# Optimization experiments

Hardware: AMD Instinct MI355X
Metric: run time of the kernel (lower is better)

Reference implementation:

```python
import jax, jax.numpy as jnp
import numpy as np

NUM_BINS = 100
EPS = 1e-6  # F.pairwise_distance default eps (added to the difference)


def setup_inputs() -> dict:
    key = jax.random.key(0)
    k0, k1, k2 = jax.random.split(key, 3)
    n, c, h, w = 1, 32, 1024, 1024
    # scale so per-pixel L2 distances (~sqrt(2c)*0.05 ~ 0.4) fall inside histc's [0,1]
    feat_t0 = jax.random.normal(k0, (n, c, h, w), dtype=jnp.float32) * 0.05
    feat_t1 = jax.random.normal(k1, (n, c, h, w), dtype=jnp.float32) * 0.05
    ground_truth = jax.random.randint(k2, (n, h, w), 0, 2, dtype=jnp.int32)
    return {"feat_t0": feat_t0, "feat_t1": feat_t1, "ground_truth": ground_truth}


def _masked_hist(d, mask):
    # torch.histc(x, bins=100, min=0, max=1): values outside [0,1] ignored,
    # right edge (==1) goes into last bin.
    in_range = (d >= 0.0) & (d <= 1.0)
    bins = jnp.clip(jnp.floor(d * NUM_BINS).astype(jnp.int32), 0, NUM_BINS - 1)
    wts = (mask & in_range).astype(d.dtype)
    return jnp.zeros((NUM_BINS,), d.dtype).at[bins].add(wts)


def reference(feat_t0, feat_t1, ground_truth):
    n, c, h, w = feat_t0.shape
    # view(c, h*w).T -> [h*w, c] pixel vectors (matches original's n=1 assumption)
    x0 = feat_t0.reshape(c, h * w).T
    x1 = feat_t1.reshape(c, h * w).T
    # F.pairwise_distance p=2: ||x0 - x1 + eps||_2 over channel dim -> [h*w]
    d = jnp.sqrt(jnp.sum((x0 - x1 + EPS) ** 2, axis=1))

    gt = ground_truth.reshape(h * w)
    pos_mask = gt == 0
    neg_mask = jnp.logical_not(pos_mask)
    pos_size = jnp.sum(pos_mask).astype(d.dtype)
    neg_size = jnp.sum(neg_mask).astype(d.dtype)

    hist_pos = _masked_hist(d, pos_mask) / pos_size
    hist_neg = _masked_hist(d, neg_mask) / neg_size

    # F.kl_div(input=hist_pos, target=hist_neg), reduction='mean':
    # mean over bins of target*(log(target) - input); target==0 contributes 0.
    pointwise = jnp.where(hist_neg > 0,
                          hist_neg * (jnp.log(jnp.where(hist_neg > 0, hist_neg, 1.0)) - hist_pos),
                          0.0)
    kl = jnp.mean(pointwise)
    loss = 1.0 + kl  # dist = 1.0/1 + kl
    return loss
```

## Files before the change

kernel.cpp:

```cpp
#include <hip/hip_runtime.h>
#include <math.h>

#define NUM_BINS 100
#define EPS 1e-6f

#define WS_WORDS (2 * NUM_BINS + 1)

#define NREP 8
#define SH_POSC (2 * NUM_BINS * NREP)
#define SH_WORDS (SH_POSC + 1)

typedef float  vfloat4 __attribute__((ext_vector_type(4)));
typedef int    vint4   __attribute__((ext_vector_type(4)));

__global__ void hml_init_ws(unsigned int* __restrict__ ws) {
    int i = blockIdx.x * blockDim.x + threadIdx.x;
    if (i < WS_WORDS) ws[i] = 0u;
}

__global__ __launch_bounds__(256) void hml_hist32(
    const vfloat4* __restrict__ f0v, const vfloat4* __restrict__ f1v,
    const vint4* __restrict__ gt, unsigned int* __restrict__ ws, int hw4)
{
    __shared__ unsigned int sh[SH_WORDS];
    for (int i = threadIdx.x; i < SH_WORDS; i += 256) sh[i] = 0u;
    __syncthreads();

    const int idx = blockIdx.x * 256 + threadIdx.x;
    const int col = threadIdx.x & (NREP - 1);

    vint4 g = __builtin_nontemporal_load(&gt[idx]);
    float s0 = 0.f, s1 = 0.f, s2 = 0.f, s3 = 0.f;

    #pragma unroll 1
    for (int cg = 0; cg < 32; cg += 4) {
        vfloat4 a[4], b[4];
        #pragma unroll
        for (int j = 0; j < 4; ++j)
            a[j] = __builtin_nontemporal_load(&f0v[(size_t)(cg + j) * hw4 + idx]);
        #pragma unroll
        for (int j = 0; j < 4; ++j)
            b[j] = __builtin_nontemporal_load(&f1v[(size_t)(cg + j) * hw4 + idx]);
        #pragma unroll
        for (int j = 0; j < 4; ++j) {
            float e0 = a[j].x - b[j].x + EPS;
            float e1 = a[j].y - b[j].y + EPS;
            float e2 = a[j].z - b[j].z + EPS;
            float e3 = a[j].w - b[j].w + EPS;
            s0 = fmaf(e0, e0, s0);
            s1 = fmaf(e1, e1, s1);
            s2 = fmaf(e2, e2, s2);
            s3 = fmaf(e3, e3, s3);
        }
    }

    float d[4] = { sqrtf(s0), sqrtf(s1), sqrtf(s2), sqrtf(s3) };
    int gg[4] = { g.x, g.y, g.z, g.w };

    int posc = (gg[0] == 0) + (gg[1] == 0) + (gg[2] == 0) + (gg[3] == 0);
    for (int off = 32; off > 0; off >>= 1)
        posc += __shfl_down(posc, off, 64);
    if ((threadIdx.x & 63) == 0 && posc)
        atomicAdd(&sh[SH_POSC], (unsigned)posc);

    #pragma unroll
    for (int k = 0; k < 4; ++k) {
        float dd = d[k];
        if (dd <= 1.0f) {
            int bin = (int)(dd * (float)NUM_BINS);
            if (bin > NUM_BINS - 1) bin = NUM_BINS - 1;
            int logical = bin + ((gg[k] != 0) ? NUM_BINS : 0);
            atomicAdd(&sh[logical * NREP + col], 1u);
        }
    }

    __syncthreads();
    {
        int i = threadIdx.x;
        if (i < 2 * NUM_BINS) {
            unsigned v = 0;
            #pragma unroll
            for (int c = 0; c < NREP; ++c) v += sh[i * NREP + c];
            if (v) atomicAdd(&ws[i], v);
        } else if (i == 2 * NUM_BINS) {
            unsigned v = sh[SH_POSC];
            if (v) atomicAdd(&ws[2 * NUM_BINS], v);
        }
    }
}

__global__ __launch_bounds__(256) void hml_hist_generic(
    const float* __restrict__ f0, const float* __restrict__ f1,
    const int* __restrict__ gt, unsigned int* __restrict__ ws,
    int hw, int C)
{
    __shared__ unsigned int sh[WS_WORDS];
    for (int i = threadIdx.x; i < WS_WORDS; i += blockDim.x) sh[i] = 0u;
    __syncthreads();

    const int hw4 = hw >> 2;
    const int idx = blockIdx.x * blockDim.x + threadIdx.x;

    if (idx < hw4) {
        const float4* __restrict__ f0v = (const float4*)f0;
        const float4* __restrict__ f1v = (const float4*)f1;
        float s0 = 0.f, s1 = 0.f, s2 = 0.f, s3 = 0.f;
        for (int c = 0; c < C; ++c) {
            float4 a = f0v[(size_t)c * hw4 + idx];
            float4 b = f1v[(size_t)c * hw4 + idx];
            float e0 = a.x - b.x + EPS, e1 = a.y - b.y + EPS;
            float e2 = a.z - b.z + EPS, e3 = a.w - b.w + EPS;
            s0 = fmaf(e0, e0, s0); s1 = fmaf(e1, e1, s1);
            s2 = fmaf(e2, e2, s2); s3 = fmaf(e3, e3, s3);
        }
        int4 g = ((const int4*)gt)[idx];
        float d[4] = { sqrtf(s0), sqrtf(s1), sqrtf(s2), sqrtf(s3) };
        int gg[4] = { g.x, g.y, g.z, g.w };
        int posc = 0;
        #pragma unroll
        for (int k = 0; k < 4; ++k) {
            posc += (gg[k] == 0) ? 1 : 0;
            float dd = d[k];
            if (dd <= 1.0f) {
                int bin = (int)(dd * (float)NUM_BINS);
                if (bin > NUM_BINS - 1) bin = NUM_BINS - 1;
                atomicAdd(&sh[bin + ((gg[k] != 0) ? NUM_BINS : 0)], 1u);
            }
        }
        if (posc) atomicAdd(&sh[2 * NUM_BINS], (unsigned)posc);
    }
    __syncthreads();
    for (int i = threadIdx.x; i < WS_WORDS; i += blockDim.x) {
        unsigned v = sh[i];
        if (v) atomicAdd(&ws[i], v);
    }
}

__global__ void hml_final(const unsigned int* __restrict__ ws,
                          float* __restrict__ out, int hw)
{
    __shared__ float terms[NUM_BINS];
    int i = threadIdx.x;
    unsigned pos = ws[2 * NUM_BINS];
    float pos_size = (float)pos;
    float neg_size = (float)(hw - (int)pos);
    if (i < NUM_BINS) {
        float hp = (float)ws[i] / pos_size;
        unsigned cn = ws[NUM_BINS + i];
        float hn = (float)cn / neg_size;
        terms[i] = (cn > 0u) ? hn * (logf(hn) - hp) : 0.0f;
    }
    __syncthreads();
    if (i == 0) {
        float s = 0.f;
        for (int k = 0; k < NUM_BINS; ++k) s += terms[k];
        out[0] = 1.0f + s / (float)NUM_BINS;
    }
}

extern "C" void kernel_launch(void* const* d_in, const int* in_sizes, int n_in,
                              void* d_out, int out_size, void* d_ws, size_t ws_size,
                              hipStream_t stream) {
    const float* f0 = (const float*)d_in[0];
    const float* f1 = (const float*)d_in[1];
    const int*   gt = (const int*)d_in[2];
    float* out = (float*)d_out;
    unsigned int* ws = (unsigned int*)d_ws;

    const int hw = in_sizes[2];
    const int C  = in_sizes[0] / hw;

    hml_init_ws<<<1, 256, 0, stream>>>(ws);

    if (C == 32 && (hw & 1023) == 0) {
        const int hw4 = hw >> 2;
        const int blocks = hw4 / 256;
        hml_hist32<<<blocks, 256, 0, stream>>>(
            (const vfloat4*)f0, (const vfloat4*)f1, (const vint4*)gt, ws, hw4);
    } else {
        const int hw4 = hw >> 2;
        const int blocks = (hw4 + 255) / 256;
        hml_hist_generic<<<blocks, 256, 0, stream>>>(f0, f1, gt, ws, hw, C);
    }

    hml_final<<<1, 128, 0, stream>>>(ws, out, hw);
}
```

Measured before the change: 259.7 us.

## Replace global atomics with per-block partial histograms reduced in final kernel

Each histogram block now writes its 201-word partial result to its own workspace slice instead of doing global atomicAdds on a shared histogram. The final kernel, widened to 1024 threads, sums the slices across all 1024 blocks before computing the KL term. This removes the init kernel launch and contention on the global atomics. In exchange it adds a serial reduction over about 200K words in a single block, and the workspace must be large enough to hold all slices.

```diff
diff --git a/kernel.cpp b/kernel.cpp
--- a/kernel.cpp
+++ b/kernel.cpp
@@ -4,7 +4,7 @@
 #define NUM_BINS 100
 #define EPS 1e-6f
 
-#define WS_WORDS (2 * NUM_BINS + 1)
+#define SLICE_WORDS (2 * NUM_BINS + 1)
 
 #define NREP 8
 #define SH_POSC (2 * NUM_BINS * NREP)
@@ -12,11 +12,6 @@
 
 typedef float  vfloat4 __attribute__((ext_vector_type(4)));
 typedef int    vint4   __attribute__((ext_vector_type(4)));
-
-__global__ void hml_init_ws(unsigned int* __restrict__ ws) {
-    int i = blockIdx.x * blockDim.x + threadIdx.x;
-    if (i < WS_WORDS) ws[i] = 0u;
-}
 
 __global__ __launch_bounds__(256) void hml_hist32(
     const vfloat4* __restrict__ f0v, const vfloat4* __restrict__ f1v,
@@ -77,14 +72,14 @@
     __syncthreads();
     {
         int i = threadIdx.x;
+        size_t base = (size_t)blockIdx.x * SLICE_WORDS;
         if (i < 2 * NUM_BINS) {
             unsigned v = 0;
             #pragma unroll
             for (int c = 0; c < NREP; ++c) v += sh[i * NREP + c];
-            if (v) atomicAdd(&ws[i], v);
+            ws[base + i] = v;
         } else if (i == 2 * NUM_BINS) {
-            unsigned v = sh[SH_POSC];
-            if (v) atomicAdd(&ws[2 * NUM_BINS], v);
+            ws[base + i] = sh[SH_POSC];
         }
     }
 }
@@ -94,8 +89,8 @@
     const int* __restrict__ gt, unsigned int* __restrict__ ws,
     int hw, int C)
 {
-    __shared__ unsigned int sh[WS_WORDS];
-    for (int i = threadIdx.x; i < WS_WORDS; i += blockDim.x) sh[i] = 0u;
+    __shared__ unsigned int sh[SLICE_WORDS];
+    for (int i = threadIdx.x; i < SLICE_WORDS; i += blockDim.x) sh[i] = 0u;
     __syncthreads();
 
     const int hw4 = hw >> 2;
@@ -130,28 +125,44 @@
         if (posc) atomicAdd(&sh[2 * NUM_BINS], (unsigned)posc);
     }
     __syncthreads();
-    for (int i = threadIdx.x; i < WS_WORDS; i += blockDim.x) {
-        unsigned v = sh[i];
-        if (v) atomicAdd(&ws[i], v);
-    }
+    for (int i = threadIdx.x; i < SLICE_WORDS; i += blockDim.x)
+        ws[(size_t)blockIdx.x * SLICE_WORDS + i] = sh[i];
 }
 
-__global__ void hml_final(const unsigned int* __restrict__ ws,
-                          float* __restrict__ out, int hw)
+__global__ __launch_bounds__(1024) void hml_final(
+    const unsigned int* __restrict__ ws, float* __restrict__ out,
+    int hw, int nblocks)
 {
+    __shared__ unsigned int part[4][SLICE_WORDS];
     __shared__ float terms[NUM_BINS];
-    int i = threadIdx.x;
-    unsigned pos = ws[2 * NUM_BINS];
+    const int t = threadIdx.x;
+    const int word = t & 255;
+    const int q = t >> 8;
+
+    if (word < SLICE_WORDS) {
+        unsigned acc = 0;
+        #pragma unroll 4
+        for (int b = q; b < nblocks; b += 4)
+            acc += ws[(size_t)b * SLICE_WORDS + word];
+        part[q][word] = acc;
+    }
+    __syncthreads();
+
+    if (t < SLICE_WORDS)
+        part[0][t] = part[0][t] + part[1][t] + part[2][t] + part[3][t];
+    __syncthreads();
+
+    unsigned pos = part[0][2 * NUM_BINS];
     float pos_size = (float)pos;
     float neg_size = (float)(hw - (int)pos);
-    if (i < NUM_BINS) {
-        float hp = (float)ws[i] / pos_size;
-        unsigned cn = ws[NUM_BINS + i];
+    if (t < NUM_BINS) {
+        float hp = (float)part[0][t] / pos_size;
+        unsigned cn = part[0][NUM_BINS + t];
         float hn = (float)cn / neg_size;
-        terms[i] = (cn > 0u) ? hn * (logf(hn) - hp) : 0.0f;
+        terms[t] = (cn > 0u) ? hn * (logf(hn) - hp) : 0.0f;
     }
     __syncthreads();
-    if (i == 0) {
+    if (t == 0) {
         float s = 0.f;
         for (int k = 0; k < NUM_BINS; ++k) s += terms[k];
         out[0] = 1.0f + s / (float)NUM_BINS;
@@ -170,18 +181,17 @@
     const int hw = in_sizes[2];
     const int C  = in_sizes[0] / hw;
 
-    hml_init_ws<<<1, 256, 0, stream>>>(ws);
-
+    int nblocks;
     if (C == 32 && (hw & 1023) == 0) {
         const int hw4 = hw >> 2;
-        const int blocks = hw4 / 256;
-        hml_hist32<<<blocks, 256, 0, stream>>>(
+        nblocks = hw4 / 256;
+        hml_hist32<<<nblocks, 256, 0, stream>>>(
             (const vfloat4*)f0, (const vfloat4*)f1, (const vint4*)gt, ws, hw4);
     } else {
         const int hw4 = hw >> 2;
-        const int blocks = (hw4 + 255) / 256;
-        hml_hist_generic<<<blocks, 256, 0, stream>>>(f0, f1, gt, ws, hw, C);
+        nblocks = (hw4 + 255) / 256;
+        hml_hist_generic<<<nblocks, 256, 0, stream>>>(f0, f1, gt, ws, hw, C);
     }
 
-    hml_final<<<1, 128, 0, stream>>>(ws, out, hw);
+    hml_final<<<1, 1024, 0, stream>>>(ws, out, hw, nblocks);
 }
```

After: 270.3 us. 4.1% more time.
